# Kernel tuning notes

Hardware: AMD Instinct MI355X
Metric: run time of the kernel (lower is better)

Reference implementation:

```python
import jax, jax.numpy as jnp
import numpy as np

NEG_SLOPE = 0.2
N_NODES, N_EDGES, D, R_MOL = 100000, 800000, 64, 8
N_MOL, N_RXN_EDGES, R_RXN, N_RXN = 5000, 40000, 4, 1024
DIM_HIDDEN, DIM_OUT = 512, 703
READOUT = 2 * D


def seg_softmax(scores, seg, num_seg):
    m = jax.ops.segment_max(scores, seg, num_segments=num_seg)
    m = jnp.where(jnp.isfinite(m), m, 0.0)
    ex = jnp.exp(scores - m[seg])
    s = jax.ops.segment_sum(ex, seg, num_segments=num_seg)
    return ex / (s[seg] + 1e-9)


def rgat_layer(h, src, dst, rel, W, a_src, a_dst, num_nodes):
    # h: [N, d]; W: [R, d, d]; a_*: [R, d]
    hW = jnp.einsum('nd,rde->rne', h, W)            # [R, N, d]
    att_s = jnp.einsum('rne,re->rn', hW, a_src)     # [R, N]
    att_d = jnp.einsum('rne,re->rn', hW, a_dst)
    scores = jax.nn.leaky_relu(att_s[rel, src] + att_d[rel, dst], NEG_SLOPE)  # [E]
    alpha = seg_softmax(scores, dst, num_nodes)     # [E]
    msg = alpha[:, None] * hW[rel, src]             # [E, d] gather + scale
    agg = jax.ops.segment_sum(msg, dst, num_segments=num_nodes)
    return jax.nn.elu(agg)


def setup_inputs() -> dict:
    key = jax.random.key(0)
    ks = jax.random.split(key, 24)
    s = 0.1
    inp = {
        'node_feats': jax.random.normal(ks[0], (N_NODES, D), jnp.float32),
        'edge_src': jax.random.randint(ks[1], (N_EDGES,), 0, N_NODES, jnp.int32),
        'edge_dst': jax.random.randint(ks[2], (N_EDGES,), 0, N_NODES, jnp.int32),
        'edge_rel': jax.random.randint(ks[3], (N_EDGES,), 0, R_MOL, jnp.int32),
        'node2mol': jnp.sort(jax.random.randint(ks[4], (N_NODES,), 0, N_MOL, jnp.int32)),
        'rxn_src': jax.random.randint(ks[5], (N_RXN_EDGES,), 0, N_MOL, jnp.int32),
        'rxn_dst': jax.random.randint(ks[6], (N_RXN_EDGES,), 0, N_MOL, jnp.int32),
        'rxn_rel': jax.random.randint(ks[7], (N_RXN_EDGES,), 0, R_RXN, jnp.int32),
        'mol2rxn': jnp.sort(jax.random.randint(ks[8], (N_MOL,), 0, N_RXN, jnp.int32)),
        'W1': jax.random.normal(ks[9], (R_MOL, D, D), jnp.float32) * s,
        'a_src1': jax.random.normal(ks[10], (R_MOL, D), jnp.float32) * s,
        'a_dst1': jax.random.normal(ks[11], (R_MOL, D), jnp.float32) * s,
        'W2': jax.random.normal(ks[12], (R_MOL, D, D), jnp.float32) * s,
        'a_src2': jax.random.normal(ks[13], (R_MOL, D), jnp.float32) * s,
        'a_dst2': jax.random.normal(ks[14], (R_MOL, D), jnp.float32) * s,
        'Wr': jax.random.normal(ks[15], (R_RXN, D, D), jnp.float32) * s,
        'a_srcr': jax.random.normal(ks[16], (R_RXN, D), jnp.float32) * s,
        'a_dstr': jax.random.normal(ks[17], (R_RXN, D), jnp.float32) * s,
        'w_fc1': jax.random.normal(ks[18], (READOUT, DIM_HIDDEN), jnp.float32) * s,
        'b_fc1': jnp.zeros((DIM_HIDDEN,), jnp.float32),
        'prelu1': jnp.asarray(0.25, jnp.float32),
        'w_fc2': jax.random.normal(ks[19], (DIM_HIDDEN, DIM_OUT), jnp.float32) * s,
        'b_fc2': jnp.zeros((DIM_OUT,), jnp.float32),
    }
    return inp


def reference(node_feats, edge_src, edge_dst, edge_rel, node2mol, rxn_src, rxn_dst,
              rxn_rel, mol2rxn, W1, a_src1, a_dst1, W2, a_src2, a_dst2,
              Wr, a_srcr, a_dstr, w_fc1, b_fc1, prelu1, w_fc2, b_fc2):
    # atom-level RGAT (2 layers)
    h = rgat_layer(node_feats, edge_src, edge_dst, edge_rel, W1, a_src1, a_dst1, N_NODES)
    h = rgat_layer(h, edge_src, edge_dst, edge_rel, W2, a_src2, a_dst2, N_NODES)
    # molecule readout
    mol = jax.ops.segment_sum(h, node2mol, num_segments=N_MOL)           # [M, d]
    # reaction-graph RGAT over molecule nodes
    molr = rgat_layer(mol, rxn_src, rxn_dst, rxn_rel, Wr, a_srcr, a_dstr, N_MOL)
    # reaction readout: concat attended + direct molecule sums
    rxn1 = jax.ops.segment_sum(molr, mol2rxn, num_segments=N_RXN)        # [B, d]
    rxn2 = jax.ops.segment_sum(mol, mol2rxn, num_segments=N_RXN)         # [B, d]
    feat = jnp.concatenate([rxn1, rxn2], axis=-1)                        # [B, 2d]
    # MLP head: Linear -> PReLU -> Linear
    hm = feat @ w_fc1 + b_fc1
    hm = jnp.where(hm > 0, hm, prelu1 * hm)
    return hm @ w_fc2 + b_fc2                                            # [B, 703]
```

## Files before the change

kernel.cpp:

```cpp
#include <hip/hip_runtime.h>
#include <math.h>

#define NEG_SLOPE 0.2f

typedef __attribute__((ext_vector_type(8))) short short8;
typedef __attribute__((ext_vector_type(8))) unsigned short ushort8v;
typedef __attribute__((ext_vector_type(4))) float float4v;

__device__ __forceinline__ void atomAddF(float* p, float v) {
    unsafeAtomicAdd(p, v);
}
__device__ __forceinline__ unsigned short f2bf(float f) {
    unsigned u = __float_as_uint(f);
    unsigned r = (u + 0x7FFFu + ((u >> 16) & 1u)) >> 16;
    return (unsigned short)r;
}
__device__ __forceinline__ float bf2f(unsigned short b) {
    return __uint_as_float((unsigned)b << 16);
}


__global__ void bhist_kernel(const int* __restrict__ dst, int* __restrict__ bcnt, int E) {
    __shared__ int h[256];
    int t = threadIdx.x;
    h[t] = 0;
    __syncthreads();
    for (int e = blockIdx.x * blockDim.x + t; e < E; e += gridDim.x * blockDim.x)
        atomicAdd(&h[dst[e] >> 9], 1);
    __syncthreads();
    if (h[t]) atomicAdd(&bcnt[t], h[t]);
}

__global__ void bscan_kernel(const int* __restrict__ bcnt, int* __restrict__ bbase,
                             int* __restrict__ bcursor, int NB, int* __restrict__ rowptr,
                             int n, int E) {
    __shared__ int s[256];
    int t = threadIdx.x;
    int v = (t < NB) ? bcnt[t] : 0;
    s[t] = v; __syncthreads();
    for (int o = 1; o < 256; o <<= 1) {
        int u = (t >= o) ? s[t - o] : 0;
        __syncthreads(); s[t] += u; __syncthreads();
    }
    int excl = s[t] - v;
    if (t < NB) { bbase[t] = excl; bcursor[t] = excl; }
    if (t == 0) { bbase[NB] = E; rowptr[n] = E; }
}

__global__ __launch_bounds__(256) void bpart_kernel(
        const int* __restrict__ dst, const int* __restrict__ rel, const int* __restrict__ src,
        int* __restrict__ bcursor, unsigned* __restrict__ bpacked, int E, int NB) {
    __shared__ int cntL[256];
    __shared__ int gofsL[256];
    int t = threadIdx.x;
    int e0 = blockIdx.x * 4096;
    cntL[t] = 0;
    __syncthreads();

    unsigned pv[16]; unsigned short li[16]; unsigned char bk[16];
#pragma unroll
    for (int j = 0; j < 16; j++) {
        int e = e0 + t + j * 256;
        bk[j] = 0xFF;
        if (e < E) {
            int d = dst[e];
            int b = d >> 9;
            bk[j] = (unsigned char)b;
            li[j] = (unsigned short)atomicAdd(&cntL[b], 1);
            pv[j] = ((unsigned)(d & 511) << 23) | ((unsigned)rel[e] << 19) | (unsigned)src[e];
        }
    }
    __syncthreads();
    for (int b = t; b < NB; b += 256) {
        int c = cntL[b];
        gofsL[b] = c ? atomicAdd(&bcursor[b], c) : 0;
    }
    __syncthreads();
#pragma unroll
    for (int j = 0; j < 16; j++)
        if (bk[j] != 0xFF) bpacked[gofsL[bk[j]] + li[j]] = pv[j];
}

#define BCAP 6400
__global__ __launch_bounds__(256) void bsort_kernel(
        const unsigned* __restrict__ bpacked, const int* __restrict__ bbase,
        int* __restrict__ rowptr, unsigned* __restrict__ packed, int n) {
    __shared__ unsigned ein[BCAP];
    __shared__ unsigned eout[BCAP];
    __shared__ int cnt[512];
    __shared__ int ofs[512];
    __shared__ int s2[256];
    int b = blockIdx.x, t = threadIdx.x;
    int g0 = bbase[b];
    int nb = bbase[b + 1] - g0;
    if (nb > BCAP) nb = BCAP;

    for (int i = t; i < nb; i += 256) ein[i] = bpacked[g0 + i];
    cnt[t] = 0; cnt[t + 256] = 0;
    __syncthreads();
    for (int i = t; i < nb; i += 256) atomicAdd(&cnt[ein[i] >> 23], 1);
    __syncthreads();
    int a = cnt[2 * t], c2 = cnt[2 * t + 1];
    s2[t] = a + c2;
    __syncthreads();
    for (int o = 1; o < 256; o <<= 1) {
        int u = (t >= o) ? s2[t - o] : 0;
        __syncthreads(); s2[t] += u; __syncthreads();
    }
    int excl = s2[t] - (a + c2);
    ofs[2 * t] = excl; ofs[2 * t + 1] = excl + a;
    __syncthreads();
    int d0 = b * 512;
    for (int j = t; j < 512; j += 256) {
        int gd = d0 + j;
        if (gd < n) rowptr[gd] = g0 + ofs[j];
    }
    cnt[t] = ofs[t]; cnt[t + 256] = ofs[t + 256];
    __syncthreads();
    for (int i = t; i < nb; i += 256) {
        unsigned v = ein[i];
        int pos = atomicAdd(&cnt[v >> 23], 1);
        eout[pos] = (((v >> 19) & 0xFu) << 24) | (v & 0x7FFFFu);
    }
    __syncthreads();
    for (int i = t; i < nb; i += 256) packed[g0 + i] = eout[i];
}

__global__ void compute_v_kernel(const float* __restrict__ W,
                                 const float* __restrict__ a_src,
                                 const float* __restrict__ a_dst,
                                 float* __restrict__ Vsrc, float* __restrict__ Vdst,
                                 int R) {
    int idx = blockIdx.x * blockDim.x + threadIdx.x;
    if (idx >= R * 64) return;
    int r = idx >> 6;
    const float* Wr = W + idx * 64;
    const float* as = a_src + r * 64;
    const float* ad = a_dst + r * 64;
    float s = 0.f, t = 0.f;
    for (int e = 0; e < 64; e++) { float w = Wr[e]; s = fmaf(w, as[e], s); t = fmaf(w, ad[e], t); }
    Vsrc[idx] = s; Vdst[idx] = t;
}

#define HPAD 68
__global__ __launch_bounds__(256) void att_gemm_kernel(
        const float* __restrict__ h,
        const float* __restrict__ Vsrc, const float* __restrict__ Vdst,
        float* __restrict__ attS, float* __restrict__ attD,
        int N, int R) {
    __shared__ float hl[64 * HPAD];
    __shared__ float Vs[8 * HPAD];
    __shared__ float Vd[8 * HPAD];
    int t = threadIdx.x;
    int n0 = blockIdx.x * 64;

    {
        const float4* hg = (const float4*)h;
#pragma unroll
        for (int i = 0; i < 4; i++) {
            int idx = t + i * 256;
            int row = idx >> 4, col4 = idx & 15;
            int node = n0 + row;
            float4 v = (node < N) ? hg[(size_t)node * 16 + col4] : float4{0.f, 0.f, 0.f, 0.f};
            *(float4*)&hl[row * HPAD + col4 * 4] = v;
        }
    }
    for (int i = t; i < R * 64; i += 256) {
        int r = i >> 6, d = i & 63;
        Vs[r * HPAD + d] = Vsrc[i];
        Vd[r * HPAD + d] = Vdst[i];
    }
    __syncthreads();

    for (int p = t; p < 64 * R; p += 256) {
        int node = p / R, r = p - node * R;
        const float4* hp = (const float4*)&hl[node * HPAD];
        const float4* sp = (const float4*)&Vs[r * HPAD];
        const float4* dp = (const float4*)&Vd[r * HPAD];
        float s = 0.f, dd = 0.f;
#pragma unroll
        for (int d4 = 0; d4 < 16; d4++) {
            float4 hv = hp[d4], sv = sp[d4], dv = dp[d4];
            s  = fmaf(hv.x, sv.x, s);  s  = fmaf(hv.y, sv.y, s);
            s  = fmaf(hv.z, sv.z, s);  s  = fmaf(hv.w, sv.w, s);
            dd = fmaf(hv.x, dv.x, dd); dd = fmaf(hv.y, dv.y, dd);
            dd = fmaf(hv.z, dv.z, dd); dd = fmaf(hv.w, dv.w, dd);
        }
        int gn = n0 + node;
        if (gn < N) { attS[(size_t)gn * R + r] = s; attD[(size_t)gn * R + r] = dd; }
    }
}

#define BSTRIDE 72
__global__ __launch_bounds__(256) void hw_gemm_mfma_kernel(
        const float* __restrict__ h, const float* __restrict__ W,
        unsigned short* __restrict__ hWb, int N, int r0, int r1) {
    __shared__ unsigned short hb[64 * BSTRIDE];
    __shared__ unsigned short wt[64 * BSTRIDE];
    int t = threadIdx.x;
    int n0 = blockIdx.x * 64;

    {
        const float4* hg = (const float4*)h;
#pragma unroll
        for (int i = 0; i < 4; i++) {
            int idx = t + i * 256;
            int row = idx >> 4, c4 = idx & 15;
            int node = n0 + row;
            float4 v = (node < N) ? hg[(size_t)node * 16 + c4] : float4{0.f, 0.f, 0.f, 0.f};
            ushort4 b;
            b.x = f2bf(v.x); b.y = f2bf(v.y); b.z = f2bf(v.z); b.w = f2bf(v.w);
            *(ushort4*)&hb[row * BSTRIDE + c4 * 4] = b;
        }
    }
    __syncthreads();

    int w = t >> 6, lane = t & 63;
    int quad = lane >> 4, m = lane & 15;
    int arow = w * 16 + m;
    short8 a0 = *(const short8*)&hb[arow * BSTRIDE + quad * 8];
    short8 a1 = *(const short8*)&hb[arow * BSTRIDE + 32 + quad * 8];

    for (int r = r0; r < r1; r++) {
        __syncthreads();
        {
            const float4* Wg = (const float4*)(W + (size_t)r * 4096);
#pragma unroll
            for (int i = 0; i < 4; i++) {
                int idx = t + i * 256;
                int k = idx >> 4, e4 = (idx & 15) * 4;
                float4 v = Wg[idx];
                wt[(e4 + 0) * BSTRIDE + k] = f2bf(v.x);
                wt[(e4 + 1) * BSTRIDE + k] = f2bf(v.y);
                wt[(e4 + 2) * BSTRIDE + k] = f2bf(v.z);
                wt[(e4 + 3) * BSTRIDE + k] = f2bf(v.w);
            }
        }
        __syncthreads();

        size_t outBase = ((size_t)(r - r0) * N + n0 + w * 16) * 64;
#pragma unroll
        for (int c = 0; c < 4; c++) {
            short8 b0 = *(const short8*)&wt[(c * 16 + m) * BSTRIDE + quad * 8];
            short8 b1 = *(const short8*)&wt[(c * 16 + m) * BSTRIDE + 32 + quad * 8];
            float4v acc = {0.f, 0.f, 0.f, 0.f};
            acc = __builtin_amdgcn_mfma_f32_16x16x32_bf16(a0, b0, acc, 0, 0, 0);
            acc = __builtin_amdgcn_mfma_f32_16x16x32_bf16(a1, b1, acc, 0, 0, 0);
#pragma unroll
            for (int reg = 0; reg < 4; reg++) {
                int node = n0 + w * 16 + quad * 4 + reg;
                if (node < N)
                    hWb[outBase + (size_t)(quad * 4 + reg) * 64 + c * 16 + m] = f2bf(acc[reg]);
            }
        }
    }
}

__global__ __launch_bounds__(256) void aggsoft_kernel(
        const int* __restrict__ rowptr, const unsigned* __restrict__ packed,
        const float* __restrict__ attS, const float* __restrict__ attD,
        const unsigned short* __restrict__ hWb, float* __restrict__ agg,
        int n, int N, int R, int r0, int r1, int last) {
    int g = blockIdx.x * blockDim.x + threadIdx.x;
    int wv = g >> 6, lane = g & 63;
    if (wv >= n) return;
    int start = rowptr[wv], end = rowptr[wv + 1];
    int deg = end - start;
    int egrp = lane >> 3, dgrp = lane & 7;

    float acc8[8] = {0.f, 0.f, 0.f, 0.f, 0.f, 0.f, 0.f, 0.f};
    if (r0 != 0) {
#pragma unroll
        for (int j = 0; j < 8; j += 4) {
            float4 v = *(const float4*)&agg[(size_t)wv * 64 + dgrp * 8 + j];
            acc8[j] = v.x; acc8[j + 1] = v.y; acc8[j + 2] = v.z; acc8[j + 3] = v.w;
        }
    }

    if (deg > 0 && deg <= 64) {
        int i = start + lane;
        bool act = i < end;
        unsigned p = act ? packed[i] : 0u;
        int r = p >> 24; unsigned s = p & 0xFFFFFFu;

        unsigned pp0 = (unsigned)__shfl((int)p, egrp);
        int rr0 = (int)(pp0 >> 24);
        bool g0 = (egrp < deg) && rr0 >= r0 && rr0 < r1;
        ushort8v v0 = {};
        if (g0) {
            unsigned row = (unsigned)((rr0 - r0) * N) + (pp0 & 0xFFFFFFu);
            v0 = *(const ushort8v*)&hWb[((size_t)row << 6) + dgrp * 8];
        }

        float sc = -INFINITY;
        if (act) {
            sc = attS[(size_t)s * R + r] + attD[(size_t)wv * R + r];
            sc = sc > 0.f ? sc : NEG_SLOPE * sc;
        }
        float m = sc, sum;
        if (deg <= 8) {
            for (int o = 4; o; o >>= 1) m = fmaxf(m, __shfl_xor(m, o));
            float ex = act ? __expf(sc - m) : 0.f;
            sum = ex;
            for (int o = 4; o; o >>= 1) sum += __shfl_xor(sum, o);
            sc = ex;
        } else {
            for (int o = 32; o; o >>= 1) m = fmaxf(m, __shfl_xor(m, o));
            float ex = act ? __expf(sc - m) : 0.f;
            sum = ex;
            for (int o = 32; o; o >>= 1) sum += __shfl_xor(sum, o);
            sc = ex;
        }
        float a = sc * __builtin_amdgcn_rcpf(sum + 1e-9f);
        float ag = (act && r >= r0 && r < r1) ? a : 0.f;

        {
            float aa = __shfl(ag, egrp);
            if (g0 && aa != 0.f) {
#pragma unroll
                for (int j = 0; j < 8; j++) acc8[j] = fmaf(aa, bf2f(v0[j]), acc8[j]);
            }
        }
        int nchunk = (deg + 7) >> 3;
        for (int c = 1; c < nchunk; c++) {
            int el = c * 8 + egrp;
            float aa = __shfl(ag, el);
            unsigned pp = (unsigned)__shfl((int)p, el);
            if (aa != 0.f) {
                unsigned row = (unsigned)(((pp >> 24) - r0) * (unsigned)N) + (pp & 0xFFFFFFu);
                ushort8v v = *(const ushort8v*)&hWb[((size_t)row << 6) + dgrp * 8];
#pragma unroll
                for (int j = 0; j < 8; j++) acc8[j] = fmaf(aa, bf2f(v[j]), acc8[j]);
            }
        }
#pragma unroll
        for (int msk = 8; msk <= 32; msk <<= 1)
#pragma unroll
            for (int j = 0; j < 8; j++) acc8[j] += __shfl_xor(acc8[j], msk);
    } else if (deg > 64) {
        float m = -INFINITY;
        for (int base = start; base < end; base += 64) {
            int i = base + lane;
            if (i < end) {
                unsigned p = packed[i];
                int r = p >> 24; unsigned s = p & 0xFFFFFFu;
                float sc = attS[(size_t)s * R + r] + attD[(size_t)wv * R + r];
                sc = sc > 0.f ? sc : NEG_SLOPE * sc;
                m = fmaxf(m, sc);
            }
        }
        for (int o = 32; o; o >>= 1) m = fmaxf(m, __shfl_xor(m, o));
        float sum = 0.f;
        for (int base = start; base < end; base += 64) {
            int i = base + lane;
            if (i < end) {
                unsigned p = packed[i];
                int r = p >> 24; unsigned s = p & 0xFFFFFFu;
                float sc = attS[(size_t)s * R + r] + attD[(size_t)wv * R + r];
                sc = sc > 0.f ? sc : NEG_SLOPE * sc;
                sum += __expf(sc - m);
            }
        }
        for (int o = 32; o; o >>= 1) sum += __shfl_xor(sum, o);
        float inv = __builtin_amdgcn_rcpf(sum + 1e-9f);
        int nchunk = (deg + 7) >> 3;
        for (int c = 0; c < nchunk; c++) {
            int el = c * 8 + egrp;
            if (el < deg) {
                unsigned p = packed[start + el];
                int r = p >> 24; unsigned s = p & 0xFFFFFFu;
                if (r >= r0 && r < r1) {
                    float sc = attS[(size_t)s * R + r] + attD[(size_t)wv * R + r];
                    sc = sc > 0.f ? sc : NEG_SLOPE * sc;
                    float aa = __expf(sc - m) * inv;
                    unsigned row = (unsigned)((r - r0) * N) + s;
                    ushort8v v = *(const ushort8v*)&hWb[((size_t)row << 6) + dgrp * 8];
#pragma unroll
                    for (int j = 0; j < 8; j++) acc8[j] = fmaf(aa, bf2f(v[j]), acc8[j]);
                }
            }
        }
#pragma unroll
        for (int msk = 8; msk <= 32; msk <<= 1)
#pragma unroll
            for (int j = 0; j < 8; j++) acc8[j] += __shfl_xor(acc8[j], msk);
    }

    if (last) {
#pragma unroll
        for (int j = 0; j < 8; j++)
            acc8[j] = acc8[j] > 0.f ? acc8[j] : (__expf(acc8[j]) - 1.f);
    }
    if (egrp == 0) {
        float4 v0 = {acc8[0], acc8[1], acc8[2], acc8[3]};
        float4 v1 = {acc8[4], acc8[5], acc8[6], acc8[7]};
        *(float4*)&agg[(size_t)wv * 64 + dgrp * 8] = v0;
        *(float4*)&agg[(size_t)wv * 64 + dgrp * 8 + 4] = v1;
    }
}

__global__ void seg_sum64_kernel(const float* __restrict__ h, const int* __restrict__ seg,
                                 float* __restrict__ out, int N) {
    int i = blockIdx.x * blockDim.x + threadIdx.x;
    if (i >= N * 64) return;
    int n = i >> 6, d = i & 63;
    atomAddF(&out[seg[n] * 64 + d], h[i]);
}

__global__ void readout_kernel(const float* __restrict__ molr, const float* __restrict__ mol,
                               const int* __restrict__ mol2rxn, float* __restrict__ feat, int M) {
    int i = blockIdx.x * blockDim.x + threadIdx.x;
    if (i >= M * 64) return;
    int m = i >> 6, d = i & 63;
    int b = mol2rxn[m];
    atomAddF(&feat[b * 128 + d], molr[i]);
    atomAddF(&feat[b * 128 + 64 + d], mol[i]);
}

#define APAD 36
__global__ __launch_bounds__(256) void fc_gemm_kernel(
        const float* __restrict__ A, const float* __restrict__ B,
        const float* __restrict__ bias, const float* __restrict__ prelu,
        float* __restrict__ C, int M, int N, int K, int mode) {
    __shared__ float Al[64 * APAD];
    __shared__ float Bl[32 * 64];
    int t = threadIdx.x;
    int n0 = blockIdx.x * 64, m0 = blockIdx.y * 64;
    int e4 = (t & 15) * 4;
    int n4 = (t >> 4) * 4;
    float acc[4][4] = {};

    for (int k0 = 0; k0 < K; k0 += 32) {
        {
            const float4* Ag = (const float4*)A;
#pragma unroll
            for (int i = 0; i < 2; i++) {
                int idx = t + i * 256;
                int row = idx >> 3, c4 = idx & 7;
                float4 v = Ag[(size_t)(m0 + row) * (K >> 2) + (k0 >> 2) + c4];
                float* p = &Al[row * APAD + c4 * 4];
                p[0] = v.x; p[1] = v.y; p[2] = v.z; p[3] = v.w;
            }
        }
        {
#pragma unroll
            for (int i = 0; i < 2; i++) {
                int idx = t + i * 256;
                int kk = idx >> 4, c4 = (idx & 15) * 4;
                int col = n0 + c4;
                float4 v;
                const float* Brow = B + (size_t)(k0 + kk) * N;
                if (col + 3 < N) v = *(const float4*)&Brow[col];
                else {
                    v.x = (col + 0 < N) ? Brow[col + 0] : 0.f;
                    v.y = (col + 1 < N) ? Brow[col + 1] : 0.f;
                    v.z = (col + 2 < N) ? Brow[col + 2] : 0.f;
                    v.w = 0.f;
                }
                *(float4*)&Bl[kk * 64 + c4] = v;
            }
        }
        __syncthreads();
        for (int d = 0; d < 32; d += 4) {
            float4 wv[4], hv[4];
#pragma unroll
            for (int dd = 0; dd < 4; dd++) wv[dd] = *(const float4*)&Bl[(d + dd) * 64 + e4];
#pragma unroll
            for (int i = 0; i < 4; i++) hv[i] = *(const float4*)&Al[(n4 + i) * APAD + d];
#pragma unroll
            for (int i = 0; i < 4; i++) {
                const float hvv[4] = {hv[i].x, hv[i].y, hv[i].z, hv[i].w};
#pragma unroll
                for (int dd = 0; dd < 4; dd++) {
                    const float* wp = (const float*)&wv[dd];
#pragma unroll
                    for (int j = 0; j < 4; j++) acc[i][j] = fmaf(hvv[dd], wp[j], acc[i][j]);
                }
            }
        }
        __syncthreads();
    }

    float p = mode ? *prelu : 0.f;
#pragma unroll
    for (int i = 0; i < 4; i++) {
        int row = m0 + n4 + i;
#pragma unroll
        for (int j = 0; j < 4; j++) {
            int col = n0 + e4 + j;
            if (col < N) {
                float v = acc[i][j] + bias[col];
                if (mode) v = v > 0.f ? v : p * v;
                C[(size_t)row * N + col] = v;
            }
        }
    }
}

extern "C" void kernel_launch(void* const* d_in, const int* in_sizes, int n_in,
                              void* d_out, int out_size, void* d_ws, size_t ws_size,
                              hipStream_t stream) {
    const float* node_feats = (const float*)d_in[0];
    const int*   edge_src   = (const int*)d_in[1];
    const int*   edge_dst   = (const int*)d_in[2];
    const int*   edge_rel   = (const int*)d_in[3];
    const int*   node2mol   = (const int*)d_in[4];
    const int*   rxn_src    = (const int*)d_in[5];
    const int*   rxn_dst    = (const int*)d_in[6];
    const int*   rxn_rel    = (const int*)d_in[7];
    const int*   mol2rxn    = (const int*)d_in[8];
    const float* W1     = (const float*)d_in[9];
    const float* a_src1 = (const float*)d_in[10];
    const float* a_dst1 = (const float*)d_in[11];
    const float* W2     = (const float*)d_in[12];
    const float* a_src2 = (const float*)d_in[13];
    const float* a_dst2 = (const float*)d_in[14];
    const float* Wr     = (const float*)d_in[15];
    const float* a_srcr = (const float*)d_in[16];
    const float* a_dstr = (const float*)d_in[17];
    const float* w_fc1  = (const float*)d_in[18];
    const float* b_fc1  = (const float*)d_in[19];
    const float* prelu1 = (const float*)d_in[20];
    const float* w_fc2  = (const float*)d_in[21];
    const float* b_fc2  = (const float*)d_in[22];

    const int N = 100000, E = 800000, M = 5000, ER = 40000;

    float* ws = (float*)d_ws;
    float* h1     = ws;
    float* h2     = h1 + 6400000;
    float* attS   = h2 + 6400000;
    float* attD   = attS + 800000;
    float* mol    = attD + 800000;
    float* molr   = mol + 320000;
    float* feat   = molr + 320000;
    float* hm     = feat + 131072;
    float* Vsrc   = hm + 524288;
    float* Vdst   = Vsrc + 512;
    int* rowptr   = (int*)(Vdst + 512);
    int* bcnt     = rowptr + 100008;
    int* bbase    = bcnt + 256;
    int* bcursor  = bbase + 260;
    unsigned* bpacked = (unsigned*)(bcursor + 256);
    unsigned* packed  = bpacked + 800000;
    unsigned short* hWb = (unsigned short*)(packed + 800000);

    size_t usedBytes = (size_t)((char*)hWb - (char*)d_ws);
    size_t availUshorts = (ws_size > usedBytes) ? (ws_size - usedBytes) / 2 : 0;

    auto buildCSR = [&](const int* dstArr, const int* srcArr, const int* relArr, int n, int e) {
        int NB = (n + 511) / 512;
        hipMemsetAsync(bcnt, 0, (size_t)NB * sizeof(int), stream);
        bhist_kernel<<<dim3(256), 256, 0, stream>>>(dstArr, bcnt, e);
        bscan_kernel<<<dim3(1), 256, 0, stream>>>(bcnt, bbase, bcursor, NB, rowptr, n, e);
        bpart_kernel<<<dim3((e + 4095) / 4096), 256, 0, stream>>>(dstArr, relArr, srcArr, bcursor, bpacked, e, NB);
        bsort_kernel<<<dim3(NB), 256, 0, stream>>>(bpacked, bbase, rowptr, packed, n);
    };

    auto rgat = [&](const float* hin, int n,
                    const float* W, const float* as, const float* ad,
                    float* agg, int R) {
        compute_v_kernel<<<dim3((R * 64 + 63) / 64), 64, 0, stream>>>(W, as, ad, Vsrc, Vdst, R);
        att_gemm_kernel<<<dim3((n + 63) / 64), 256, 0, stream>>>(hin, Vsrc, Vdst, attS, attD, n, R);

        size_t perRel = (size_t)n * 64;
        int chunk = (int)(availUshorts / perRel);
        if (chunk < 1) chunk = 1;
        if (chunk > R) chunk = R;
        for (int r0 = 0; r0 < R; r0 += chunk) {
            int r1 = r0 + chunk; if (r1 > R) r1 = R;
            hw_gemm_mfma_kernel<<<dim3((n + 63) / 64), 256, 0, stream>>>(hin, W, hWb, n, r0, r1);
            aggsoft_kernel<<<dim3(((size_t)n * 64 + 255) / 256), 256, 0, stream>>>(
                rowptr, packed, attS, attD, hWb, agg, n, n, R, r0, r1, r1 == R ? 1 : 0);
        }
    };

    buildCSR(edge_dst, edge_src, edge_rel, N, E);
    rgat(node_feats, N, W1, a_src1, a_dst1, h1, 8);
    rgat(h1,         N, W2, a_src2, a_dst2, h2, 8);

    hipMemsetAsync(mol, 0, (size_t)M * 64 * sizeof(float), stream);
    seg_sum64_kernel<<<dim3(((size_t)N * 64 + 255) / 256), 256, 0, stream>>>(h2, node2mol, mol, N);

    buildCSR(rxn_dst, rxn_src, rxn_rel, M, ER);
    rgat(mol, M, Wr, a_srcr, a_dstr, molr, 4);

    hipMemsetAsync(feat, 0, (size_t)1024 * 128 * sizeof(float), stream);
    readout_kernel<<<dim3(((size_t)M * 64 + 255) / 256), 256, 0, stream>>>(molr, mol, mol2rxn, feat, M);

    fc_gemm_kernel<<<dim3(8, 16), 256, 0, stream>>>(feat, w_fc1, b_fc1, prelu1, hm, 1024, 512, 128, 1);
    fc_gemm_kernel<<<dim3(11, 16), 256, 0, stream>>>(hm, w_fc2, b_fc2, nullptr, (float*)d_out, 1024, 703, 512, 0);
}
```

Before: 508.4 us.

## Fuse attention projections into MFMA hW GEMM and store layer-1 output as bf16

The separate att_gemm pass is removed. The attention projections h·Vsrc and h·Vdst are now computed with extra MFMA ops inside hw_gemm_mfma_kernel, using a zero-padded bf16 V matrix whose first two columns hold Vsrc and Vdst. This drops one full read of h per layer and one kernel launch. Layer 1 now writes its ELU output as bf16, so layer 2 reads half the bytes. In exchange, the attention scores and the layer-2 input lose precision to bf16 rounding, and a slower scalar fallback runs when relations must be chunked.

```diff
diff --git a/kernel.cpp b/kernel.cpp
--- a/kernel.cpp
+++ b/kernel.cpp
@@ -18,7 +18,6 @@
 __device__ __forceinline__ float bf2f(unsigned short b) {
     return __uint_as_float((unsigned)b << 16);
 }
-
 
 __global__ void bhist_kernel(const int* __restrict__ dst, int* __restrict__ bcnt, int E) {
     __shared__ int h[256];
@@ -129,79 +128,65 @@
 __global__ void compute_v_kernel(const float* __restrict__ W,
                                  const float* __restrict__ a_src,
                                  const float* __restrict__ a_dst,
-                                 float* __restrict__ Vsrc, float* __restrict__ Vdst,
-                                 int R) {
+                                 unsigned short* __restrict__ Vbpad, int R) {
     int idx = blockIdx.x * blockDim.x + threadIdx.x;
     if (idx >= R * 64) return;
-    int r = idx >> 6;
+    int r = idx >> 6, d = idx & 63;
     const float* Wr = W + idx * 64;
     const float* as = a_src + r * 64;
     const float* ad = a_dst + r * 64;
     float s = 0.f, t = 0.f;
     for (int e = 0; e < 64; e++) { float w = Wr[e]; s = fmaf(w, as[e], s); t = fmaf(w, ad[e], t); }
-    Vsrc[idx] = s; Vdst[idx] = t;
-}
-
-#define HPAD 68
-__global__ __launch_bounds__(256) void att_gemm_kernel(
-        const float* __restrict__ h,
-        const float* __restrict__ Vsrc, const float* __restrict__ Vdst,
-        float* __restrict__ attS, float* __restrict__ attD,
-        int N, int R) {
-    __shared__ float hl[64 * HPAD];
-    __shared__ float Vs[8 * HPAD];
-    __shared__ float Vd[8 * HPAD];
-    int t = threadIdx.x;
-    int n0 = blockIdx.x * 64;
-
-    {
-        const float4* hg = (const float4*)h;
-#pragma unroll
-        for (int i = 0; i < 4; i++) {
-            int idx = t + i * 256;
-            int row = idx >> 4, col4 = idx & 15;
-            int node = n0 + row;
-            float4 v = (node < N) ? hg[(size_t)node * 16 + col4] : float4{0.f, 0.f, 0.f, 0.f};
-            *(float4*)&hl[row * HPAD + col4 * 4] = v;
-        }
-    }
-    for (int i = t; i < R * 64; i += 256) {
-        int r = i >> 6, d = i & 63;
-        Vs[r * HPAD + d] = Vsrc[i];
-        Vd[r * HPAD + d] = Vdst[i];
-    }
-    __syncthreads();
-
-    for (int p = t; p < 64 * R; p += 256) {
-        int node = p / R, r = p - node * R;
-        const float4* hp = (const float4*)&hl[node * HPAD];
-        const float4* sp = (const float4*)&Vs[r * HPAD];
-        const float4* dp = (const float4*)&Vd[r * HPAD];
-        float s = 0.f, dd = 0.f;
-#pragma unroll
-        for (int d4 = 0; d4 < 16; d4++) {
-            float4 hv = hp[d4], sv = sp[d4], dv = dp[d4];
-            s  = fmaf(hv.x, sv.x, s);  s  = fmaf(hv.y, sv.y, s);
-            s  = fmaf(hv.z, sv.z, s);  s  = fmaf(hv.w, sv.w, s);
-            dd = fmaf(hv.x, dv.x, dd); dd = fmaf(hv.y, dv.y, dd);
-            dd = fmaf(hv.z, dv.z, dd); dd = fmaf(hv.w, dv.w, dd);
-        }
-        int gn = n0 + node;
-        if (gn < N) { attS[(size_t)gn * R + r] = s; attD[(size_t)gn * R + r] = dd; }
-    }
+    Vbpad[(size_t)r * 1024 + d] = f2bf(s);
+    Vbpad[(size_t)r * 1024 + 64 + d] = f2bf(t);
+}
+
+__global__ void att_fallback_kernel(const void* __restrict__ h, int hBf16,
+                                    const unsigned short* __restrict__ Vbpad,
+                                    float* __restrict__ attS, float* __restrict__ attD,
+                                    int n, int R) {
+    int idx = blockIdx.x * blockDim.x + threadIdx.x;
+    if (idx >= n * R) return;
+    int node = idx / R, r = idx - node * R;
+    float s = 0.f, dd = 0.f;
+    for (int d = 0; d < 64; d++) {
+        float hv = hBf16 ? bf2f(((const unsigned short*)h)[(size_t)node * 64 + d])
+                         : ((const float*)h)[(size_t)node * 64 + d];
+        s  = fmaf(hv, bf2f(Vbpad[(size_t)r * 1024 + d]), s);
+        dd = fmaf(hv, bf2f(Vbpad[(size_t)r * 1024 + 64 + d]), dd);
+    }
+    attS[(size_t)node * R + r] = s;
+    attD[(size_t)node * R + r] = dd;
 }
 
 #define BSTRIDE 72
 __global__ __launch_bounds__(256) void hw_gemm_mfma_kernel(
-        const float* __restrict__ h, const float* __restrict__ W,
-        unsigned short* __restrict__ hWb, int N, int r0, int r1) {
+        const void* __restrict__ hIn, int hBf16, const float* __restrict__ W,
+        const unsigned short* __restrict__ Vbpad,
+        unsigned short* __restrict__ hWb, float* __restrict__ attS, float* __restrict__ attD,
+        int N, int R, int r0, int r1, int doAtt) {
     __shared__ unsigned short hb[64 * BSTRIDE];
     __shared__ unsigned short wt[64 * BSTRIDE];
     int t = threadIdx.x;
     int n0 = blockIdx.x * 64;
 
-    {
-        const float4* hg = (const float4*)h;
+    if (hBf16) {
+        const unsigned short* hg = (const unsigned short*)hIn;
+#pragma unroll
+        for (int i = 0; i < 2; i++) {
+            int idx = t + i * 256;
+            int row = idx >> 3, c8 = (idx & 7) * 8;
+            int node = n0 + row;
+            ushort4 v0 = {0, 0, 0, 0}, v1 = {0, 0, 0, 0};
+            if (node < N) {
+                v0 = *(const ushort4*)&hg[(size_t)node * 64 + c8];
+                v1 = *(const ushort4*)&hg[(size_t)node * 64 + c8 + 4];
+            }
+            *(ushort4*)&hb[row * BSTRIDE + c8] = v0;
+            *(ushort4*)&hb[row * BSTRIDE + c8 + 4] = v1;
+        }
+    } else {
+        const float4* hg = (const float4*)hIn;
 #pragma unroll
         for (int i = 0; i < 4; i++) {
             int idx = t + i * 256;
@@ -220,6 +205,7 @@
     int arow = w * 16 + m;
     short8 a0 = *(const short8*)&hb[arow * BSTRIDE + quad * 8];
     short8 a1 = *(const short8*)&hb[arow * BSTRIDE + 32 + quad * 8];
+    int nodeBase = n0 + w * 16 + quad * 4;
 
     for (int r = r0; r < r1; r++) {
         __syncthreads();
@@ -248,9 +234,25 @@
             acc = __builtin_amdgcn_mfma_f32_16x16x32_bf16(a1, b1, acc, 0, 0, 0);
 #pragma unroll
             for (int reg = 0; reg < 4; reg++) {
-                int node = n0 + w * 16 + quad * 4 + reg;
+                int node = nodeBase + reg;
                 if (node < N)
                     hWb[outBase + (size_t)(quad * 4 + reg) * 64 + c * 16 + m] = f2bf(acc[reg]);
+            }
+        }
+        if (doAtt) {
+            const unsigned short* Vp = Vbpad + (size_t)r * 1024;
+            short8 v0 = *(const short8*)&Vp[m * 64 + quad * 8];
+            short8 v1 = *(const short8*)&Vp[m * 64 + 32 + quad * 8];
+            float4v av = {0.f, 0.f, 0.f, 0.f};
+            av = __builtin_amdgcn_mfma_f32_16x16x32_bf16(a0, v0, av, 0, 0, 0);
+            av = __builtin_amdgcn_mfma_f32_16x16x32_bf16(a1, v1, av, 0, 0, 0);
+            if (m < 2) {
+                float* o = (m == 0) ? attS : attD;
+#pragma unroll
+                for (int reg = 0; reg < 4; reg++) {
+                    int node = nodeBase + reg;
+                    if (node < N) o[(size_t)node * R + r] = av[reg];
+                }
             }
         }
     }
@@ -260,6 +262,7 @@
         const int* __restrict__ rowptr, const unsigned* __restrict__ packed,
         const float* __restrict__ attS, const float* __restrict__ attD,
         const unsigned short* __restrict__ hWb, float* __restrict__ agg,
+        unsigned short* __restrict__ hbOut,
         int n, int N, int R, int r0, int r1, int last) {
     int g = blockIdx.x * blockDim.x + threadIdx.x;
     int wv = g >> 6, lane = g & 63;
@@ -390,8 +393,21 @@
 #pragma unroll
         for (int j = 0; j < 8; j++)
             acc8[j] = acc8[j] > 0.f ? acc8[j] : (__expf(acc8[j]) - 1.f);
-    }
-    if (egrp == 0) {
+        if (egrp == 0) {
+            if (hbOut) {
+                ushort4 o0, o1;
+                o0.x = f2bf(acc8[0]); o0.y = f2bf(acc8[1]); o0.z = f2bf(acc8[2]); o0.w = f2bf(acc8[3]);
+                o1.x = f2bf(acc8[4]); o1.y = f2bf(acc8[5]); o1.z = f2bf(acc8[6]); o1.w = f2bf(acc8[7]);
+                *(ushort4*)&hbOut[(size_t)wv * 64 + dgrp * 8] = o0;
+                *(ushort4*)&hbOut[(size_t)wv * 64 + dgrp * 8 + 4] = o1;
+            } else {
+                float4 v0 = {acc8[0], acc8[1], acc8[2], acc8[3]};
+                float4 v1 = {acc8[4], acc8[5], acc8[6], acc8[7]};
+                *(float4*)&agg[(size_t)wv * 64 + dgrp * 8] = v0;
+                *(float4*)&agg[(size_t)wv * 64 + dgrp * 8 + 4] = v1;
+            }
+        }
+    } else if (egrp == 0) {
         float4 v0 = {acc8[0], acc8[1], acc8[2], acc8[3]};
         float4 v1 = {acc8[4], acc8[5], acc8[6], acc8[7]};
         *(float4*)&agg[(size_t)wv * 64 + dgrp * 8] = v0;
@@ -527,17 +543,16 @@
     const int N = 100000, E = 800000, M = 5000, ER = 40000;
 
     float* ws = (float*)d_ws;
-    float* h1     = ws;
-    float* h2     = h1 + 6400000;
+    unsigned short* hb1 = (unsigned short*)ws;
+    float* h2     = (float*)(hb1 + 6400000);
     float* attS   = h2 + 6400000;
     float* attD   = attS + 800000;
     float* mol    = attD + 800000;
     float* molr   = mol + 320000;
     float* feat   = molr + 320000;
     float* hm     = feat + 131072;
-    float* Vsrc   = hm + 524288;
-    float* Vdst   = Vsrc + 512;
-    int* rowptr   = (int*)(Vdst + 512);
+    unsigned short* Vbpad = (unsigned short*)(hm + 524288);
+    int* rowptr   = (int*)(Vbpad + 8192);
     int* bcnt     = rowptr + 100008;
     int* bbase    = bcnt + 256;
     int* bcursor  = bbase + 260;
@@ -557,33 +572,38 @@
         bsort_kernel<<<dim3(NB), 256, 0, stream>>>(bpacked, bbase, rowptr, packed, n);
     };
 
-    auto rgat = [&](const float* hin, int n,
+    auto rgat = [&](const void* hin, int hBf16, int n,
                     const float* W, const float* as, const float* ad,
-                    float* agg, int R) {
-        compute_v_kernel<<<dim3((R * 64 + 63) / 64), 64, 0, stream>>>(W, as, ad, Vsrc, Vdst, R);
-        att_gemm_kernel<<<dim3((n + 63) / 64), 256, 0, stream>>>(hin, Vsrc, Vdst, attS, attD, n, R);
+                    float* agg, unsigned short* hbOut, int R) {
+        hipMemsetAsync(Vbpad, 0, (size_t)R * 1024 * 2, stream);
+        compute_v_kernel<<<dim3((R * 64 + 63) / 64), 64, 0, stream>>>(W, as, ad, Vbpad, R);
 
         size_t perRel = (size_t)n * 64;
         int chunk = (int)(availUshorts / perRel);
         if (chunk < 1) chunk = 1;
         if (chunk > R) chunk = R;
+        int fused = (chunk == R) ? 1 : 0;
+        if (!fused)
+            att_fallback_kernel<<<dim3((n * R + 255) / 256), 256, 0, stream>>>(
+                hin, hBf16, Vbpad, attS, attD, n, R);
         for (int r0 = 0; r0 < R; r0 += chunk) {
             int r1 = r0 + chunk; if (r1 > R) r1 = R;
-            hw_gemm_mfma_kernel<<<dim3((n + 63) / 64), 256, 0, stream>>>(hin, W, hWb, n, r0, r1);
+            hw_gemm_mfma_kernel<<<dim3((n + 63) / 64), 256, 0, stream>>>(
+                hin, hBf16, W, Vbpad, hWb, attS, attD, n, R, r0, r1, fused);
             aggsoft_kernel<<<dim3(((size_t)n * 64 + 255) / 256), 256, 0, stream>>>(
-                rowptr, packed, attS, attD, hWb, agg, n, n, R, r0, r1, r1 == R ? 1 : 0);
+                rowptr, packed, attS, attD, hWb, agg, hbOut, n, n, R, r0, r1, r1 == R ? 1 : 0);
         }
     };
 
     buildCSR(edge_dst, edge_src, edge_rel, N, E);
-    rgat(node_feats, N, W1, a_src1, a_dst1, h1, 8);
-    rgat(h1,         N, W2, a_src2, a_dst2, h2, 8);
+    rgat(node_feats, 0, N, W1, a_src1, a_dst1, h2, hb1, 8);
+    rgat(hb1, 1, N, W2, a_src2, a_dst2, h2, nullptr, 8);
 
     hipMemsetAsync(mol, 0, (size_t)M * 64 * sizeof(float), stream);
     seg_sum64_kernel<<<dim3(((size_t)N * 64 + 255) / 256), 256, 0, stream>>>(h2, node2mol, mol, N);
 
     buildCSR(rxn_dst, rxn_src, rxn_rel, M, ER);
-    rgat(mol, M, Wr, a_srcr, a_dstr, molr, 4);
+    rgat(mol, 0, M, Wr, a_srcr, a_dstr, molr, nullptr, 4);
 
     hipMemsetAsync(feat, 0, (size_t)1024 * 128 * sizeof(float), stream);
     readout_kernel<<<dim3(((size_t)M * 64 + 255) / 256), 256, 0, stream>>>(molr, mol, mol2rxn, feat, M);
```

Measured after the change: 509.7 us. About the same (+0.2%).
